# Kernel tuning notes

Hardware: AMD Instinct MI355X
Metric: run time of the kernel (lower is better)

## Reference

```python
import jax, jax.numpy as jnp
import numpy as np

B, N, D, Kp = 32, 4096, 128, 256  # batch*heads, seq_len, head_dim, linformer proj dim


def setup_inputs() -> dict:
    key = jax.random.key(0)
    ks = jax.random.split(key, 7)
    return {
        "Q": jax.random.normal(ks[0], (B, N, D), dtype=jnp.float32),
        "K": jax.random.normal(ks[1], (B, N, D), dtype=jnp.float32),
        "V": jax.random.normal(ks[2], (B, N, D), dtype=jnp.float32),
        "E_W": jax.random.normal(ks[3], (Kp, N), dtype=jnp.float32) * (1.0 / np.sqrt(N)),
        "E_b": jax.random.normal(ks[4], (Kp,), dtype=jnp.float32) * 0.02,
        "F_W": jax.random.normal(ks[5], (Kp, N), dtype=jnp.float32) * (1.0 / np.sqrt(N)),
        "F_b": jax.random.normal(ks[6], (Kp,), dtype=jnp.float32) * 0.02,
    }


def reference(Q, K, V, E_W, E_b, F_W, F_b):
    d = Q.shape[-1]
    scale = 1.0 / jnp.sqrt(jnp.asarray(d, Q.dtype))
    # E projection on K^T: [B,d,n] @ W^T -> [B,d,k]
    K_proj = jnp.einsum('bnd,kn->bdk', K, E_W) + E_b  # bias broadcasts over k axis
    # scaled scores [B,n,k], softmax over projected dim k
    scores = jnp.einsum('bnd,bdk->bnk', Q, K_proj) * scale
    P_bar = jax.nn.softmax(scores, axis=-1)
    # F projection on V^T then transpose back: [B,k,d]
    V_proj = jnp.einsum('bnd,kn->bkd', V, F_W) + F_b[:, None]
    # [B,n,k] @ [B,k,d] -> [B,n,d]
    return jnp.einsum('bnk,bkd->bnd', P_bar, V_proj)
```

## Files before the change

### kernel.cpp

```cpp
#include <hip/hip_runtime.h>
#include <cstdint>
#include <cstddef>

#define N_SEQ 4096
#define D_HEAD 128
#define KP_DIM 256

typedef __attribute__((ext_vector_type(4))) float f32x4;
typedef __attribute__((ext_vector_type(8))) short bf16x8;
typedef __attribute__((ext_vector_type(4))) short s16x4;
typedef __attribute__((ext_vector_type(2))) unsigned int u32x2;

static __device__ __forceinline__ short f2bf(float f) {
  uint32_t u = __builtin_bit_cast(uint32_t, f);
  u += 0x7FFFu + ((u >> 16) & 1u);
  return (short)(u >> 16);
}

static __device__ __forceinline__ unsigned int cvtpk(float a, float b) {
  unsigned int r;
  asm("v_cvt_pk_bf16_f32 %0, %1, %2" : "=v"(r) : "v"(a), "v"(b));
  return r;
}

static __device__ __forceinline__ int swz8(int r) { return (r ^ (r >> 2)) & 7; }

__global__ __launch_bounds__(256) void conv_w_kernel(
    const float* __restrict__ EW, const float* __restrict__ FW,
    short* __restrict__ wbf) {
  const int idx = blockIdx.x * 256 + threadIdx.x;
  const int half = 262144;
  f32x4 v = (idx < half) ? *(const f32x4*)(EW + (size_t)idx * 4)
                         : *(const f32x4*)(FW + (size_t)(idx - half) * 4);
  u32x2 h = {cvtpk(v[0], v[1]), cvtpk(v[2], v[3])};
  *(u32x2*)(wbf + (size_t)idx * 4) = h;
}

__global__ __launch_bounds__(512) void proj_partial_kernel(
    const float* __restrict__ Kin, const float* __restrict__ Vin,
    const short* __restrict__ wbf, float* __restrict__ pws) {
  const int bid = blockIdx.x;
  const int wk = (bid & 7) * 32 + (bid >> 3);
  const int b = wk & 31;
  const int s = (wk >> 5) & 3;
  const int p = wk >> 7;

  const float* __restrict__ X = (p == 0 ? Kin : Vin) + (size_t)b * (N_SEQ * D_HEAD);
  const short* __restrict__ wp = wbf + (size_t)p * (KP_DIM * N_SEQ);
  float* __restrict__ outp = pws + ((((size_t)b * 2 + p) * 4) + s) * (KP_DIM * D_HEAD);

  __shared__ __align__(16) short lw[2][KP_DIM * 64];
  __shared__ __align__(16) short xt[2][D_HEAD * 64];

  const int t = threadIdx.x;
  const int lane = t & 63;
  const int w = t >> 6;
  const int wm = (w >> 1) * 64;
  const int wn = (w & 1) * 64;
  const int l15 = lane & 15;
  const int l4 = lane >> 4;
  const int dq = t & 31;
  const int ng = t >> 5;

  const int n0 = s * 1024;

  f32x4 acc[4][4];
#pragma unroll
  for (int i = 0; i < 4; ++i)
#pragma unroll
    for (int j = 0; j < 4; ++j) acc[i][j] = (f32x4){0.f, 0.f, 0.f, 0.f};

  f32x4 xreg[4];

#pragma unroll
  for (int i = 0; i < 4; ++i)
    xreg[i] = *(const f32x4*)(X + (size_t)(n0 + ng * 4 + i) * D_HEAD + dq * 4);
#pragma unroll
  for (int i = 0; i < 4; ++i) {
    int g = t + i * 512;
    int row = g >> 3, c = g & 7;
    __builtin_amdgcn_global_load_lds(
        (const __attribute__((address_space(1))) void*)(wp + (size_t)row * N_SEQ + n0 +
                                                        ((c ^ swz8(row)) << 3)),
        (__attribute__((address_space(3))) void*)(&lw[0][g * 8]), 16, 0, 0);
  }
  asm volatile("s_waitcnt vmcnt(4)" ::: "memory");
#pragma unroll
  for (int j = 0; j < 4; ++j) {
    int drow = dq * 4 + j;
    u32x2 hv = {cvtpk(xreg[0][j], xreg[1][j]), cvtpk(xreg[2][j], xreg[3][j])};
    *(u32x2*)(&xt[0][drow * 64 + ((ng * 4) ^ (swz8(drow) << 3))]) = hv;
  }
  asm volatile("s_waitcnt vmcnt(0)" ::: "memory");
  __syncthreads();

  for (int it = 0; it < 16; ++it) {
    const int cur = it & 1, nxt = cur ^ 1;
    if (it < 15) {
      const int nc = n0 + (it + 1) * 64;
#pragma unroll
      for (int i = 0; i < 4; ++i)
        xreg[i] = *(const f32x4*)(X + (size_t)(nc + ng * 4 + i) * D_HEAD + dq * 4);
#pragma unroll
      for (int i = 0; i < 4; ++i) {
        int g = t + i * 512;
        int row = g >> 3, c = g & 7;
        __builtin_amdgcn_global_load_lds(
            (const __attribute__((address_space(1))) void*)(wp + (size_t)row * N_SEQ + nc +
                                                            ((c ^ swz8(row)) << 3)),
            (__attribute__((address_space(3))) void*)(&lw[nxt][g * 8]), 16, 0, 0);
      }
    }
#pragma unroll
    for (int ks2 = 0; ks2 < 2; ++ks2) {
      const int col0 = ks2 * 32 + l4 * 8;
      bf16x8 a[4], bb[4];
#pragma unroll
      for (int mt = 0; mt < 4; ++mt) {
        int row = wm + mt * 16 + l15;
        a[mt] = *(const bf16x8*)(&lw[cur][row * 64 + (col0 ^ (swz8(row) << 3))]);
      }
#pragma unroll
      for (int nt = 0; nt < 4; ++nt) {
        int row = wn + nt * 16 + l15;
        bb[nt] = *(const bf16x8*)(&xt[cur][row * 64 + (col0 ^ (swz8(row) << 3))]);
      }
#pragma unroll
      for (int mt = 0; mt < 4; ++mt)
#pragma unroll
        for (int nt = 0; nt < 4; ++nt)
          acc[mt][nt] = __builtin_amdgcn_mfma_f32_16x16x32_bf16(a[mt], bb[nt], acc[mt][nt], 0, 0, 0);
    }
    if (it < 15) {
      asm volatile("s_waitcnt vmcnt(4)" ::: "memory");
#pragma unroll
      for (int j = 0; j < 4; ++j) {
        int drow = dq * 4 + j;
        u32x2 hv = {cvtpk(xreg[0][j], xreg[1][j]), cvtpk(xreg[2][j], xreg[3][j])};
        *(u32x2*)(&xt[nxt][drow * 64 + ((ng * 4) ^ (swz8(drow) << 3))]) = hv;
      }
      asm volatile("s_waitcnt vmcnt(0)" ::: "memory");
    }
    __syncthreads();
  }

#pragma unroll
  for (int mt = 0; mt < 4; ++mt)
#pragma unroll
    for (int nt = 0; nt < 4; ++nt)
#pragma unroll
      for (int r = 0; r < 4; ++r) {
        int kk = wm + mt * 16 + l4 * 4 + r;
        int dd = wn + nt * 16 + l15;
        outp[kk * D_HEAD + dd] = acc[mt][nt][r];
      }
}

__global__ __launch_bounds__(256) void reduce_bias_kernel(
    const float* __restrict__ pws, const float* __restrict__ Eb,
    const float* __restrict__ Fb, short* __restrict__ kp, short* __restrict__ vpt) {
  const int sub = blockIdx.x & 3;
  const int b = blockIdx.x >> 2;
  const int t = threadIdx.x;
  __shared__ short tile[128 * 128];
  if (sub < 2) {
    const float* __restrict__ base = pws + ((size_t)b * 2) * 4 * 32768;
    const int off = sub * 16384;
    for (int i = t; i < 16384; i += 256) {
      int ii = off + i;
      int k = ii >> 7;
      float v = base[ii] + base[ii + 32768] + base[ii + 65536] + base[ii + 98304] + Eb[k];
      kp[(size_t)b * 32768 + ii] = f2bf(v);
    }
  } else {
    const int kh = sub - 2;
    const float* __restrict__ base = pws + (((size_t)b * 2 + 1) * 4) * 32768 + kh * 16384;
    for (int i = t; i < 16384; i += 256) {
      int kl = i >> 7, d = i & 127;
      float v = base[i] + base[i + 32768] + base[i + 65536] + base[i + 98304] + Fb[kh * 128 + kl];
      tile[kl * 128 + (d ^ ((kl & 15) << 3))] = f2bf(v);
    }
    __syncthreads();
    for (int i = t; i < 16384; i += 256) {
      int d = i >> 7, kl = i & 127;
      vpt[(size_t)b * 32768 + d * 256 + kh * 128 + kl] = tile[kl * 128 + (d ^ ((kl & 15) << 3))];
    }
  }
}

__global__ __launch_bounds__(1024, 4) void attn_kernel(
    const float* __restrict__ Q, const short* __restrict__ kp,
    const short* __restrict__ vpt, float* __restrict__ out) {
  const int bid = blockIdx.x;
  const int wk = (bid & 7) * 32 + (bid >> 3);
  const int b = wk >> 3;
  const int slice = wk & 7;
  const int t = threadIdx.x;
  const int lane = t & 63;
  const int w = t >> 6;
  const int l15 = lane & 15, l4 = lane >> 4;

  __shared__ __align__(16) short lbuf[81920];
  short* lkp = lbuf;
  short* lvpt = lbuf + 32768;
  short* lpw = lbuf + 65536 + w * 1024;

  const short* __restrict__ kpb = kp + (size_t)b * 32768;
  const short* __restrict__ vptb = vpt + (size_t)b * 32768;

#pragma unroll
  for (int i = 0; i < 4; ++i) {
    int g = t + i * 1024;
    int row = g >> 4, c = g & 15;
    __builtin_amdgcn_global_load_lds(
        (const __attribute__((address_space(1))) void*)(kpb + (size_t)row * 128 +
                                                        ((c ^ (row & 7)) << 3)),
        (__attribute__((address_space(3))) void*)(&lkp[g * 8]), 16, 0, 0);
  }
#pragma unroll
  for (int i = 0; i < 4; ++i) {
    int g = t + i * 1024;
    int row = g >> 5, c = g & 31;
    __builtin_amdgcn_global_load_lds(
        (const __attribute__((address_space(1))) void*)(vptb + (size_t)row * 256 +
                                                        ((c ^ (row & 7)) << 3)),
        (__attribute__((address_space(3))) void*)(&lvpt[g * 8]), 16, 0, 0);
  }

  const float scale = 0.08838834764831845f;
  f32x4 qraw[8];
  {
    const float* qr = Q + ((size_t)b * N_SEQ + slice * 512 + w * 16 + l15) * D_HEAD;
#pragma unroll
    for (int ks = 0; ks < 4; ++ks) {
      qraw[2 * ks] = *(const f32x4*)(qr + ks * 32 + l4 * 8);
      qraw[2 * ks + 1] = *(const f32x4*)(qr + ks * 32 + l4 * 8 + 4);
    }
  }
  asm volatile("s_waitcnt vmcnt(0)" ::: "memory");
  __syncthreads();

#pragma unroll
  for (int rd = 0; rd < 2; ++rd) {
    const int rowBase = slice * 512 + rd * 256 + w * 16;

    bf16x8 qf[4];
#pragma unroll
    for (int ks = 0; ks < 4; ++ks) {
      union { unsigned int u[4]; bf16x8 v; } cv;
      cv.u[0] = cvtpk(qraw[2 * ks][0] * scale, qraw[2 * ks][1] * scale);
      cv.u[1] = cvtpk(qraw[2 * ks][2] * scale, qraw[2 * ks][3] * scale);
      cv.u[2] = cvtpk(qraw[2 * ks + 1][0] * scale, qraw[2 * ks + 1][1] * scale);
      cv.u[3] = cvtpk(qraw[2 * ks + 1][2] * scale, qraw[2 * ks + 1][3] * scale);
      qf[ks] = cv.v;
    }

    f32x4 accs[16];
#pragma unroll
    for (int i = 0; i < 16; ++i) accs[i] = (f32x4){0.f, 0.f, 0.f, 0.f};
#pragma unroll
    for (int ks = 0; ks < 4; ++ks) {
#pragma unroll
      for (int nt = 0; nt < 16; ++nt) {
        bf16x8 af = *(const bf16x8*)(&lkp[(nt * 16 + l15) * 128 +
                                          (((ks * 4 + l4) ^ (l15 & 7)) << 3)]);
        accs[nt] = __builtin_amdgcn_mfma_f32_16x16x32_bf16(af, qf[ks], accs[nt], 0, 0, 0);
      }
    }

    float m = -1e30f;
#pragma unroll
    for (int nt = 0; nt < 16; ++nt)
#pragma unroll
      for (int r = 0; r < 4; ++r) m = fmaxf(m, accs[nt][r]);
    m = fmaxf(m, __shfl_xor(m, 16));
    m = fmaxf(m, __shfl_xor(m, 32));
    float s = 0.f;
#pragma unroll
    for (int nt = 0; nt < 16; ++nt)
#pragma unroll
      for (int r = 0; r < 4; ++r) {
        float e = __expf(accs[nt][r] - m);
        accs[nt][r] = e;
        s += e;
      }
    s += __shfl_xor(s, 16);
    s += __shfl_xor(s, 32);
    float inv = 1.0f / s;

    f32x4 acco[8];
#pragma unroll
    for (int i = 0; i < 8; ++i) acco[i] = (f32x4){0.f, 0.f, 0.f, 0.f};
#pragma unroll
    for (int qq = 0; qq < 4; ++qq) {
#pragma unroll
      for (int ntl = 0; ntl < 4; ++ntl) {
        int nt = qq * 4 + ntl;
        int cw = 2 * ntl + (l4 >> 1);
        unsigned int p0 = cvtpk(accs[nt][0] * inv, accs[nt][1] * inv);
        unsigned int p1 = cvtpk(accs[nt][2] * inv, accs[nt][3] * inv);
        *(u32x2*)((char*)lpw + l15 * 128 + ((cw ^ (l15 & 7)) << 4) + (l4 & 1) * 8) =
            (u32x2){p0, p1};
      }
      if (rd == 0 && qq == 3) {
        const float* qr = Q + ((size_t)b * N_SEQ + slice * 512 + 256 + w * 16 + l15) * D_HEAD;
#pragma unroll
        for (int ks = 0; ks < 4; ++ks) {
          qraw[2 * ks] = *(const f32x4*)(qr + ks * 32 + l4 * 8);
          qraw[2 * ks + 1] = *(const f32x4*)(qr + ks * 32 + l4 * 8 + 4);
        }
      }
#pragma unroll
      for (int ksl = 0; ksl < 2; ++ksl) {
        bf16x8 pa = *(const bf16x8*)((char*)lpw + l15 * 128 +
                                     (((4 * ksl + l4) ^ (l15 & 7)) << 4));
        int ksa = qq * 2 + ksl;
#pragma unroll
        for (int ntv = 0; ntv < 8; ++ntv) {
          bf16x8 av = *(const bf16x8*)(&lvpt[(ntv * 16 + l15) * 256 +
                                             (((ksa * 4 + l4) ^ (l15 & 7)) << 3)]);
          acco[ntv] = __builtin_amdgcn_mfma_f32_16x16x32_bf16(av, pa, acco[ntv], 0, 0, 0);
        }
      }
    }

    float* ob = out + ((size_t)b * N_SEQ + rowBase) * D_HEAD;
#pragma unroll
    for (int ntv = 0; ntv < 8; ++ntv)
      *(f32x4*)(ob + (size_t)l15 * D_HEAD + ntv * 16 + l4 * 4) = acco[ntv];
  }
}

extern "C" void kernel_launch(void* const* d_in, const int* in_sizes, int n_in,
                              void* d_out, int out_size, void* d_ws, size_t ws_size,
                              hipStream_t stream) {
  const float* Q  = (const float*)d_in[0];
  const float* K  = (const float*)d_in[1];
  const float* V  = (const float*)d_in[2];
  const float* EW = (const float*)d_in[3];
  const float* Eb = (const float*)d_in[4];
  const float* FW = (const float*)d_in[5];
  const float* Fb = (const float*)d_in[6];
  float* out = (float*)d_out;

  short* wbf = (short*)d_out;
  float* pws = (float*)d_out + 2097152;
  short* kpb = (short*)d_ws;
  short* vpt = (short*)((char*)d_ws + (size_t)32 * KP_DIM * D_HEAD * 2);

  conv_w_kernel<<<dim3(2048), dim3(256), 0, stream>>>(EW, FW, wbf);
  proj_partial_kernel<<<dim3(256), dim3(512), 0, stream>>>(K, V, wbf, pws);
  reduce_bias_kernel<<<dim3(128), dim3(256), 0, stream>>>(pws, Eb, Fb, kpb, vpt);
  attn_kernel<<<dim3(256), dim3(1024), 0, stream>>>(Q, kpb, vpt, out);
}
```

Baseline: 97.53 us.

## Replace split-N projection plus reduce kernel with full-N output-tiled projection

The projection kernel no longer splits the sequence dimension into four partial sums that a separate reduce kernel adds up. Each block now owns a 64x64 output tile (k quarter, d half) and loops over the full N, then adds the bias, converts to bf16 and writes K_proj or the transposed V_proj directly. This removes the fp32 partial-sum round trip through global memory and one kernel launch. In exchange each block does more serial iterations with smaller tiles. K/V and the weights are also reloaded once per tile, so more redundant global reads happen and the transposed V output uses strided stores.

```diff
diff --git a/kernel.cpp b/kernel.cpp
--- a/kernel.cpp
+++ b/kernel.cpp
@@ -36,55 +36,56 @@
   *(u32x2*)(wbf + (size_t)idx * 4) = h;
 }
 
-__global__ __launch_bounds__(512) void proj_partial_kernel(
+__global__ __launch_bounds__(256, 4) void proj_full_kernel(
     const float* __restrict__ Kin, const float* __restrict__ Vin,
-    const short* __restrict__ wbf, float* __restrict__ pws) {
+    const short* __restrict__ wbf, const float* __restrict__ Eb,
+    const float* __restrict__ Fb, short* __restrict__ kp,
+    short* __restrict__ vpt) {
   const int bid = blockIdx.x;
-  const int wk = (bid & 7) * 32 + (bid >> 3);
-  const int b = wk & 31;
-  const int s = (wk >> 5) & 3;
-  const int p = wk >> 7;
+  const int wk = (bid & 7) * 64 + (bid >> 3);
+  const int kq = wk & 3;
+  const int dh = (wk >> 2) & 1;
+  const int b  = (wk >> 3) & 31;
+  const int p  = (wk >> 8) & 1;
 
   const float* __restrict__ X = (p == 0 ? Kin : Vin) + (size_t)b * (N_SEQ * D_HEAD);
-  const short* __restrict__ wp = wbf + (size_t)p * (KP_DIM * N_SEQ);
-  float* __restrict__ outp = pws + ((((size_t)b * 2 + p) * 4) + s) * (KP_DIM * D_HEAD);
-
-  __shared__ __align__(16) short lw[2][KP_DIM * 64];
-  __shared__ __align__(16) short xt[2][D_HEAD * 64];
+  const short* __restrict__ wp =
+      wbf + (size_t)p * (KP_DIM * N_SEQ) + (size_t)(kq * 64) * N_SEQ;
+
+  __shared__ __align__(16) short lw[2][64 * 64];
+  __shared__ __align__(16) short xt[2][64 * 64];
 
   const int t = threadIdx.x;
   const int lane = t & 63;
   const int w = t >> 6;
-  const int wm = (w >> 1) * 64;
-  const int wn = (w & 1) * 64;
+  const int wkk = (w >> 1) * 32;
+  const int wdd = (w & 1) * 32;
   const int l15 = lane & 15;
   const int l4 = lane >> 4;
-  const int dq = t & 31;
-  const int ng = t >> 5;
-
-  const int n0 = s * 1024;
-
-  f32x4 acc[4][4];
+  const int dq = t & 15;
+  const int ng = t >> 4;
+
+  f32x4 acc[2][2];
+#pragma unroll
+  for (int i = 0; i < 2; ++i)
+#pragma unroll
+    for (int j = 0; j < 2; ++j) acc[i][j] = (f32x4){0.f, 0.f, 0.f, 0.f};
+
+  f32x4 xreg[4];
+
 #pragma unroll
   for (int i = 0; i < 4; ++i)
-#pragma unroll
-    for (int j = 0; j < 4; ++j) acc[i][j] = (f32x4){0.f, 0.f, 0.f, 0.f};
-
-  f32x4 xreg[4];
-
-#pragma unroll
-  for (int i = 0; i < 4; ++i)
-    xreg[i] = *(const f32x4*)(X + (size_t)(n0 + ng * 4 + i) * D_HEAD + dq * 4);
-#pragma unroll
-  for (int i = 0; i < 4; ++i) {
-    int g = t + i * 512;
+    xreg[i] = *(const f32x4*)(X + (size_t)(ng * 4 + i) * D_HEAD + dh * 64 + dq * 4);
+#pragma unroll
+  for (int i = 0; i < 2; ++i) {
+    int g = t + i * 256;
     int row = g >> 3, c = g & 7;
     __builtin_amdgcn_global_load_lds(
-        (const __attribute__((address_space(1))) void*)(wp + (size_t)row * N_SEQ + n0 +
+        (const __attribute__((address_space(1))) void*)(wp + (size_t)row * N_SEQ +
                                                         ((c ^ swz8(row)) << 3)),
         (__attribute__((address_space(3))) void*)(&lw[0][g * 8]), 16, 0, 0);
   }
-  asm volatile("s_waitcnt vmcnt(4)" ::: "memory");
+  asm volatile("s_waitcnt vmcnt(2)" ::: "memory");
 #pragma unroll
   for (int j = 0; j < 4; ++j) {
     int drow = dq * 4 + j;
@@ -94,16 +95,16 @@
   asm volatile("s_waitcnt vmcnt(0)" ::: "memory");
   __syncthreads();
 
-  for (int it = 0; it < 16; ++it) {
+  for (int it = 0; it < 64; ++it) {
     const int cur = it & 1, nxt = cur ^ 1;
-    if (it < 15) {
-      const int nc = n0 + (it + 1) * 64;
+    if (it < 63) {
+      const int nc = (it + 1) * 64;
 #pragma unroll
       for (int i = 0; i < 4; ++i)
-        xreg[i] = *(const f32x4*)(X + (size_t)(nc + ng * 4 + i) * D_HEAD + dq * 4);
-#pragma unroll
-      for (int i = 0; i < 4; ++i) {
-        int g = t + i * 512;
+        xreg[i] = *(const f32x4*)(X + (size_t)(nc + ng * 4 + i) * D_HEAD + dh * 64 + dq * 4);
+#pragma unroll
+      for (int i = 0; i < 2; ++i) {
+        int g = t + i * 256;
         int row = g >> 3, c = g & 7;
         __builtin_amdgcn_global_load_lds(
             (const __attribute__((address_space(1))) void*)(wp + (size_t)row * N_SEQ + nc +
@@ -111,28 +112,51 @@
             (__attribute__((address_space(3))) void*)(&lw[nxt][g * 8]), 16, 0, 0);
       }
     }
-#pragma unroll
-    for (int ks2 = 0; ks2 < 2; ++ks2) {
-      const int col0 = ks2 * 32 + l4 * 8;
-      bf16x8 a[4], bb[4];
-#pragma unroll
-      for (int mt = 0; mt < 4; ++mt) {
-        int row = wm + mt * 16 + l15;
-        a[mt] = *(const bf16x8*)(&lw[cur][row * 64 + (col0 ^ (swz8(row) << 3))]);
-      }
-#pragma unroll
-      for (int nt = 0; nt < 4; ++nt) {
-        int row = wn + nt * 16 + l15;
-        bb[nt] = *(const bf16x8*)(&xt[cur][row * 64 + (col0 ^ (swz8(row) << 3))]);
-      }
-#pragma unroll
-      for (int mt = 0; mt < 4; ++mt)
-#pragma unroll
-        for (int nt = 0; nt < 4; ++nt)
-          acc[mt][nt] = __builtin_amdgcn_mfma_f32_16x16x32_bf16(a[mt], bb[nt], acc[mt][nt], 0, 0, 0);
-    }
-    if (it < 15) {
-      asm volatile("s_waitcnt vmcnt(4)" ::: "memory");
+    if (p == 0) {
+#pragma unroll
+      for (int ks = 0; ks < 2; ++ks) {
+        const int col0 = ks * 32 + l4 * 8;
+        bf16x8 a[2], bb[2];
+#pragma unroll
+        for (int mt = 0; mt < 2; ++mt) {
+          int row = wkk + mt * 16 + l15;
+          a[mt] = *(const bf16x8*)(&lw[cur][row * 64 + (col0 ^ (swz8(row) << 3))]);
+        }
+#pragma unroll
+        for (int nt = 0; nt < 2; ++nt) {
+          int row = wdd + nt * 16 + l15;
+          bb[nt] = *(const bf16x8*)(&xt[cur][row * 64 + (col0 ^ (swz8(row) << 3))]);
+        }
+#pragma unroll
+        for (int mt = 0; mt < 2; ++mt)
+#pragma unroll
+          for (int nt = 0; nt < 2; ++nt)
+            acc[mt][nt] = __builtin_amdgcn_mfma_f32_16x16x32_bf16(a[mt], bb[nt], acc[mt][nt], 0, 0, 0);
+      }
+    } else {
+#pragma unroll
+      for (int ks = 0; ks < 2; ++ks) {
+        const int col0 = ks * 32 + l4 * 8;
+        bf16x8 a[2], bb[2];
+#pragma unroll
+        for (int mt = 0; mt < 2; ++mt) {
+          int row = wkk + mt * 16 + l15;
+          a[mt] = *(const bf16x8*)(&lw[cur][row * 64 + (col0 ^ (swz8(row) << 3))]);
+        }
+#pragma unroll
+        for (int nt = 0; nt < 2; ++nt) {
+          int row = wdd + nt * 16 + l15;
+          bb[nt] = *(const bf16x8*)(&xt[cur][row * 64 + (col0 ^ (swz8(row) << 3))]);
+        }
+#pragma unroll
+        for (int mt = 0; mt < 2; ++mt)
+#pragma unroll
+          for (int nt = 0; nt < 2; ++nt)
+            acc[mt][nt] = __builtin_amdgcn_mfma_f32_16x16x32_bf16(bb[nt], a[mt], acc[mt][nt], 0, 0, 0);
+      }
+    }
+    if (it < 63) {
+      asm volatile("s_waitcnt vmcnt(2)" ::: "memory");
 #pragma unroll
       for (int j = 0; j < 4; ++j) {
         int drow = dq * 4 + j;
@@ -144,46 +168,33 @@
     __syncthreads();
   }
 
-#pragma unroll
-  for (int mt = 0; mt < 4; ++mt)
-#pragma unroll
-    for (int nt = 0; nt < 4; ++nt)
-#pragma unroll
-      for (int r = 0; r < 4; ++r) {
-        int kk = wm + mt * 16 + l4 * 4 + r;
-        int dd = wn + nt * 16 + l15;
-        outp[kk * D_HEAD + dd] = acc[mt][nt][r];
-      }
-}
-
-__global__ __launch_bounds__(256) void reduce_bias_kernel(
-    const float* __restrict__ pws, const float* __restrict__ Eb,
-    const float* __restrict__ Fb, short* __restrict__ kp, short* __restrict__ vpt) {
-  const int sub = blockIdx.x & 3;
-  const int b = blockIdx.x >> 2;
-  const int t = threadIdx.x;
-  __shared__ short tile[128 * 128];
-  if (sub < 2) {
-    const float* __restrict__ base = pws + ((size_t)b * 2) * 4 * 32768;
-    const int off = sub * 16384;
-    for (int i = t; i < 16384; i += 256) {
-      int ii = off + i;
-      int k = ii >> 7;
-      float v = base[ii] + base[ii + 32768] + base[ii + 65536] + base[ii + 98304] + Eb[k];
-      kp[(size_t)b * 32768 + ii] = f2bf(v);
+  if (p == 0) {
+    short* __restrict__ outp = kp + (size_t)b * (KP_DIM * D_HEAD);
+#pragma unroll
+    for (int mt = 0; mt < 2; ++mt) {
+      f32x4 bv = *(const f32x4*)(Eb + kq * 64 + wkk + mt * 16 + l4 * 4);
+#pragma unroll
+      for (int nt = 0; nt < 2; ++nt)
+#pragma unroll
+        for (int r = 0; r < 4; ++r) {
+          int k = kq * 64 + wkk + mt * 16 + l4 * 4 + r;
+          int d = dh * 64 + wdd + nt * 16 + l15;
+          outp[(size_t)k * D_HEAD + d] = f2bf(acc[mt][nt][r] + bv[r]);
+        }
     }
   } else {
-    const int kh = sub - 2;
-    const float* __restrict__ base = pws + (((size_t)b * 2 + 1) * 4) * 32768 + kh * 16384;
-    for (int i = t; i < 16384; i += 256) {
-      int kl = i >> 7, d = i & 127;
-      float v = base[i] + base[i + 32768] + base[i + 65536] + base[i + 98304] + Fb[kh * 128 + kl];
-      tile[kl * 128 + (d ^ ((kl & 15) << 3))] = f2bf(v);
-    }
-    __syncthreads();
-    for (int i = t; i < 16384; i += 256) {
-      int d = i >> 7, kl = i & 127;
-      vpt[(size_t)b * 32768 + d * 256 + kh * 128 + kl] = tile[kl * 128 + (d ^ ((kl & 15) << 3))];
+    short* __restrict__ outp = vpt + (size_t)b * (KP_DIM * D_HEAD);
+#pragma unroll
+    for (int mt = 0; mt < 2; ++mt) {
+      float fb = Fb[kq * 64 + wkk + mt * 16 + l15];
+#pragma unroll
+      for (int nt = 0; nt < 2; ++nt)
+#pragma unroll
+        for (int r = 0; r < 4; ++r) {
+          int d = dh * 64 + wdd + nt * 16 + l4 * 4 + r;
+          int k = kq * 64 + wkk + mt * 16 + l15;
+          outp[(size_t)d * KP_DIM + k] = f2bf(acc[mt][nt][r] + fb);
+        }
     }
   }
 }
@@ -344,12 +355,10 @@
   float* out = (float*)d_out;
 
   short* wbf = (short*)d_out;
-  float* pws = (float*)d_out + 2097152;
   short* kpb = (short*)d_ws;
   short* vpt = (short*)((char*)d_ws + (size_t)32 * KP_DIM * D_HEAD * 2);
 
   conv_w_kernel<<<dim3(2048), dim3(256), 0, stream>>>(EW, FW, wbf);
-  proj_partial_kernel<<<dim3(256), dim3(512), 0, stream>>>(K, V, wbf, pws);
-  reduce_bias_kernel<<<dim3(128), dim3(256), 0, stream>>>(pws, Eb, Fb, kpb, vpt);
+  proj_full_kernel<<<dim3(512), dim3(256), 0, stream>>>(K, V, wbf, Eb, Fb, kpb, vpt);
   attn_kernel<<<dim3(256), dim3(1024), 0, stream>>>(Q, kpb, vpt, out);
 }
```

Measured after the change: 113.0 us. 15.8% more time.

## Split projection kernel over Kp halves and read weights directly from global

Applied to the files above, without the earlier changes.

The projection kernel now splits the 256-wide projected dimension into two halves per block, doubling the grid to 512 blocks and halving per-wave accumulators. The weight tile is no longer staged in LDS via async global-to-LDS loads; each wave loads its bf16 weight fragments straight from global memory into registers. LDS use drops, and a launch bound hint allows more resident blocks. The cost is that each K/V tile is loaded and converted twice, once per half, and weight reads become uncoalesced strided global loads that rely on cache.

```diff
diff --git a/kernel.cpp b/kernel.cpp
--- a/kernel.cpp
+++ b/kernel.cpp
@@ -36,27 +36,29 @@
   *(u32x2*)(wbf + (size_t)idx * 4) = h;
 }
 
-__global__ __launch_bounds__(512) void proj_partial_kernel(
+__global__ __launch_bounds__(512, 4) void proj_partial_kernel(
     const float* __restrict__ Kin, const float* __restrict__ Vin,
     const short* __restrict__ wbf, float* __restrict__ pws) {
   const int bid = blockIdx.x;
-  const int wk = (bid & 7) * 32 + (bid >> 3);
-  const int b = wk & 31;
-  const int s = (wk >> 5) & 3;
-  const int p = wk >> 7;
+  const int wk = (bid & 7) * 64 + (bid >> 3);
+  const int kh = wk & 1;
+  const int b = (wk >> 1) & 31;
+  const int s = (wk >> 6) & 3;
+  const int p = wk >> 8;
 
   const float* __restrict__ X = (p == 0 ? Kin : Vin) + (size_t)b * (N_SEQ * D_HEAD);
-  const short* __restrict__ wp = wbf + (size_t)p * (KP_DIM * N_SEQ);
-  float* __restrict__ outp = pws + ((((size_t)b * 2 + p) * 4) + s) * (KP_DIM * D_HEAD);
-
-  __shared__ __align__(16) short lw[2][KP_DIM * 64];
+  const short* __restrict__ wp =
+      wbf + (size_t)p * (KP_DIM * N_SEQ) + (size_t)(kh * 128) * N_SEQ;
+  float* __restrict__ outp = pws + ((((size_t)b * 2 + p) * 4) + s) * (KP_DIM * D_HEAD)
+                             + (size_t)(kh * 128) * D_HEAD;
+
   __shared__ __align__(16) short xt[2][D_HEAD * 64];
 
   const int t = threadIdx.x;
   const int lane = t & 63;
   const int w = t >> 6;
-  const int wm = (w >> 1) * 64;
-  const int wn = (w & 1) * 64;
+  const int wkk = (w >> 1) * 32;
+  const int wdd = (w & 1) * 64;
   const int l15 = lane & 15;
   const int l4 = lane >> 4;
   const int dq = t & 31;
@@ -64,9 +66,9 @@
 
   const int n0 = s * 1024;
 
-  f32x4 acc[4][4];
-#pragma unroll
-  for (int i = 0; i < 4; ++i)
+  f32x4 acc[2][4];
+#pragma unroll
+  for (int i = 0; i < 2; ++i)
 #pragma unroll
     for (int j = 0; j < 4; ++j) acc[i][j] = (f32x4){0.f, 0.f, 0.f, 0.f};
 
@@ -75,83 +77,64 @@
 #pragma unroll
   for (int i = 0; i < 4; ++i)
     xreg[i] = *(const f32x4*)(X + (size_t)(n0 + ng * 4 + i) * D_HEAD + dq * 4);
-#pragma unroll
-  for (int i = 0; i < 4; ++i) {
-    int g = t + i * 512;
-    int row = g >> 3, c = g & 7;
-    __builtin_amdgcn_global_load_lds(
-        (const __attribute__((address_space(1))) void*)(wp + (size_t)row * N_SEQ + n0 +
-                                                        ((c ^ swz8(row)) << 3)),
-        (__attribute__((address_space(3))) void*)(&lw[0][g * 8]), 16, 0, 0);
-  }
-  asm volatile("s_waitcnt vmcnt(4)" ::: "memory");
+  asm volatile("s_waitcnt vmcnt(0)" ::: "memory");
 #pragma unroll
   for (int j = 0; j < 4; ++j) {
     int drow = dq * 4 + j;
     u32x2 hv = {cvtpk(xreg[0][j], xreg[1][j]), cvtpk(xreg[2][j], xreg[3][j])};
     *(u32x2*)(&xt[0][drow * 64 + ((ng * 4) ^ (swz8(drow) << 3))]) = hv;
   }
-  asm volatile("s_waitcnt vmcnt(0)" ::: "memory");
   __syncthreads();
 
   for (int it = 0; it < 16; ++it) {
     const int cur = it & 1, nxt = cur ^ 1;
+    const int nn = n0 + it * 64;
     if (it < 15) {
-      const int nc = n0 + (it + 1) * 64;
+      const int nc = nn + 64;
 #pragma unroll
       for (int i = 0; i < 4; ++i)
         xreg[i] = *(const f32x4*)(X + (size_t)(nc + ng * 4 + i) * D_HEAD + dq * 4);
-#pragma unroll
-      for (int i = 0; i < 4; ++i) {
-        int g = t + i * 512;
-        int row = g >> 3, c = g & 7;
-        __builtin_amdgcn_global_load_lds(
-            (const __attribute__((address_space(1))) void*)(wp + (size_t)row * N_SEQ + nc +
-                                                            ((c ^ swz8(row)) << 3)),
-            (__attribute__((address_space(3))) void*)(&lw[nxt][g * 8]), 16, 0, 0);
-      }
     }
 #pragma unroll
     for (int ks2 = 0; ks2 < 2; ++ks2) {
       const int col0 = ks2 * 32 + l4 * 8;
-      bf16x8 a[4], bb[4];
-#pragma unroll
-      for (int mt = 0; mt < 4; ++mt) {
-        int row = wm + mt * 16 + l15;
-        a[mt] = *(const bf16x8*)(&lw[cur][row * 64 + (col0 ^ (swz8(row) << 3))]);
+      bf16x8 a[2], bb[4];
+#pragma unroll
+      for (int mt = 0; mt < 2; ++mt) {
+        int kr = wkk + mt * 16 + l15;
+        a[mt] = *(const bf16x8*)(wp + (size_t)kr * N_SEQ + nn + col0);
       }
 #pragma unroll
       for (int nt = 0; nt < 4; ++nt) {
-        int row = wn + nt * 16 + l15;
+        int row = wdd + nt * 16 + l15;
         bb[nt] = *(const bf16x8*)(&xt[cur][row * 64 + (col0 ^ (swz8(row) << 3))]);
       }
 #pragma unroll
-      for (int mt = 0; mt < 4; ++mt)
+      for (int mt = 0; mt < 2; ++mt)
 #pragma unroll
         for (int nt = 0; nt < 4; ++nt)
           acc[mt][nt] = __builtin_amdgcn_mfma_f32_16x16x32_bf16(a[mt], bb[nt], acc[mt][nt], 0, 0, 0);
     }
     if (it < 15) {
-      asm volatile("s_waitcnt vmcnt(4)" ::: "memory");
+      asm volatile("s_waitcnt vmcnt(0)" ::: "memory");
 #pragma unroll
       for (int j = 0; j < 4; ++j) {
         int drow = dq * 4 + j;
         u32x2 hv = {cvtpk(xreg[0][j], xreg[1][j]), cvtpk(xreg[2][j], xreg[3][j])};
         *(u32x2*)(&xt[nxt][drow * 64 + ((ng * 4) ^ (swz8(drow) << 3))]) = hv;
       }
-      asm volatile("s_waitcnt vmcnt(0)" ::: "memory");
     }
     __syncthreads();
   }
 
 #pragma unroll
-  for (int mt = 0; mt < 4; ++mt)
+  for (int mt = 0; mt < 2; ++mt)
 #pragma unroll
     for (int nt = 0; nt < 4; ++nt)
 #pragma unroll
       for (int r = 0; r < 4; ++r) {
-        int kk = wm + mt * 16 + l4 * 4 + r;
-        int dd = wn + nt * 16 + l15;
+        int kk = wkk + mt * 16 + l4 * 4 + r;
+        int dd = wdd + nt * 16 + l15;
         outp[kk * D_HEAD + dd] = acc[mt][nt][r];
       }
 }
@@ -349,7 +332,7 @@
   short* vpt = (short*)((char*)d_ws + (size_t)32 * KP_DIM * D_HEAD * 2);
 
   conv_w_kernel<<<dim3(2048), dim3(256), 0, stream>>>(EW, FW, wbf);
-  proj_partial_kernel<<<dim3(256), dim3(512), 0, stream>>>(K, V, wbf, pws);
+  proj_partial_kernel<<<dim3(512), dim3(512), 0, stream>>>(K, V, wbf, pws);
   reduce_bias_kernel<<<dim3(128), dim3(256), 0, stream>>>(pws, Eb, Fb, kpb, vpt);
   attn_kernel<<<dim3(256), dim3(1024), 0, stream>>>(Q, kpb, vpt, out);
 }
```

New measurement: 114.4 us. +17.3%, slower.
